# Optimization experiments

Measured on AMD Instinct MI355X. Metric: run time of the kernel, lower is better.

## Reference

```python
import jax, jax.numpy as jnp
import numpy as np

HIDDEN = 512
B, N = 32, 96

def setup_inputs() -> dict:
    key = jax.random.key(0)
    k1, k2, k3, k4, k5 = jax.random.split(key, 5)
    h = HIDDEN
    s1 = 1.0 / np.sqrt(2 * h)
    s2 = 1.0 / np.sqrt(h)
    return {
        "encoded_sequence": jax.random.normal(k1, (B, N, h), dtype=jnp.float32),
        "W1": jax.random.uniform(k2, (h, 2 * h), dtype=jnp.float32, minval=-s1, maxval=s1),
        "b1": jax.random.uniform(k3, (h,), dtype=jnp.float32, minval=-s1, maxval=s1),
        "W2": jax.random.uniform(k4, (1, h), dtype=jnp.float32, minval=-s2, maxval=s2),
        "b2": jax.random.uniform(k5, (1,), dtype=jnp.float32, minval=-s2, maxval=s2),
    }

def reference(encoded_sequence, W1, b1, W2, b2):
    # Faithful to calc_arc_scores: arc_vectors[b,i,j] = concat(X[b,i], X[b,j]),
    # scores = Linear2(tanh(Linear1(arc_vectors))).squeeze(-1).
    # Fused (biaffine) form: split W1 into head/dep halves and broadcast-sum,
    # avoiding the O(B*n^2*2h) concatenated intermediate.
    h = W1.shape[0]
    X = encoded_sequence
    Wa = W1[:, :h]   # acts on X_i (first half of concat)
    Wb = W1[:, h:]   # acts on X_j (second half of concat)
    Ha = jnp.einsum('bnh,kh->bnk', X, Wa)            # [B, n, h]
    Hb = jnp.einsum('bnh,kh->bnk', X, Wb)            # [B, n, h]
    T = jnp.tanh(Ha[:, :, None, :] + Hb[:, None, :, :] + b1)  # [B, n, n, h]
    arc_scores = jnp.einsum('bijk,k->bij', T, W2[0]) + b2[0]   # [B, n, n]
    return arc_scores
```

## Files before the change

### kernel.cpp

```cpp
#include <hip/hip_runtime.h>
#include <hip/hip_bf16.h>

#define NN 96
#define C_TANH 2.8853900817779268f

typedef __attribute__((ext_vector_type(4))) float    f32x4;
typedef __attribute__((ext_vector_type(2))) float    f32x2;
typedef __attribute__((ext_vector_type(8))) short    short8;
typedef __attribute__((ext_vector_type(8))) _Float16 half8;

static __device__ inline unsigned int cvt_pk_bf16(float lo, float hi) {
    unsigned int r;
    asm("v_cvt_pk_bf16_f32 %0, %1, %2" : "=v"(r) : "v"(lo), "v"(hi));
    return r;
}

__global__ __launch_bounds__(256) void gemm_h(const float* __restrict__ X,
                                              const float* __restrict__ W1,
                                              const float* __restrict__ b1,
                                              _Float16* __restrict__ Ea,
                                              _Float16* __restrict__ Eh) {
    __shared__ unsigned short As[2][2048];
    __shared__ unsigned short Bs[2][2048];

    int bid  = blockIdx.x;
    int xcd  = bid & 7;
    int sub  = bid >> 3;
    int mloc = sub % 6;
    int nq   = sub / 6;
    int mb   = (xcd * 6 + mloc) * 64;
    int nb   = nq * 64;
    int tid = threadIdx.x;
    int w   = tid >> 6;
    int l   = tid & 63;

    int srow = tid >> 2;
    int sg   = (tid & 3) * 8;
    int scs  = sg ^ ((srow & 3) << 3);
    const float* asrc = X + (mb + srow) * 512 + sg;
    int nrow = nb + srow;
    const float* bsrc = W1 + (nrow & 511) * 1024 + ((nrow >> 9) << 9) + sg;
    unsigned short* adst = &As[0][srow * 32 + scs];
    unsigned short* bdst = &Bs[0][srow * 32 + scs];

    struct Regs { f32x4 a0, a1, b0, b4; };
    Regs RA, RB;

#define LOADR(R, k0)                                                          \
    {                                                                         \
        R.a0 = *(const f32x4*)(asrc + (k0));                                  \
        R.a1 = *(const f32x4*)(asrc + (k0) + 4);                              \
        R.b0 = *(const f32x4*)(bsrc + (k0));                                  \
        R.b4 = *(const f32x4*)(bsrc + (k0) + 4);                              \
    }
#define WRITER(R, buf)                                                        \
    {                                                                         \
        uint4 ua, ub;                                                         \
        ua.x = cvt_pk_bf16(R.a0[0], R.a0[1]); ua.y = cvt_pk_bf16(R.a0[2], R.a0[3]); \
        ua.z = cvt_pk_bf16(R.a1[0], R.a1[1]); ua.w = cvt_pk_bf16(R.a1[2], R.a1[3]); \
        ub.x = cvt_pk_bf16(R.b0[0], R.b0[1]); ub.y = cvt_pk_bf16(R.b0[2], R.b0[3]); \
        ub.z = cvt_pk_bf16(R.b4[0], R.b4[1]); ub.w = cvt_pk_bf16(R.b4[2], R.b4[3]); \
        *(uint4*)(adst + (buf) * 2048) = ua;                                  \
        *(uint4*)(bdst + (buf) * 2048) = ub;                                  \
    }

    int lr    = l & 15;
    int koffs = ((l >> 4) * 8) ^ ((lr & 3) << 3);
    int aoff  = (16 * w + lr) * 32 + koffs;
    int boff0 = lr * 32 + koffs;

    f32x4 acc[4] = {};

#define COMPUTE(cur)                                                          \
    {                                                                         \
        short8 afr = *(const short8*)(&As[cur][aoff]);                        \
        short8 bfr[4];                                                        \
        _Pragma("unroll")                                                     \
        for (int t = 0; t < 4; ++t)                                           \
            bfr[t] = *(const short8*)(&Bs[cur][boff0 + t * 512]);             \
        _Pragma("unroll")                                                     \
        for (int t = 0; t < 4; ++t)                                           \
            acc[t] = __builtin_amdgcn_mfma_f32_16x16x32_bf16(afr, bfr[t],     \
                                                             acc[t], 0, 0, 0);\
    }

    LOADR(RA, 0)
    WRITER(RA, 0)
    LOADR(RB, 32)
    __syncthreads();
#pragma unroll 1
    for (int kk = 0; kk < 7; ++kk) {
        LOADR(RA, (2 * kk + 2) * 32)
        COMPUTE(0)
        WRITER(RB, 1)
        __syncthreads();
        LOADR(RB, (2 * kk + 3) * 32)
        COMPUTE(1)
        WRITER(RA, 0)
        __syncthreads();
    }
    COMPUTE(0)
    WRITER(RB, 1)
    __syncthreads();
    COMPUTE(1)
#undef LOADR
#undef WRITER
#undef COMPUTE

    int r0 = (l >> 4) * 4;
    bool isB = (nb >= 512);
    int colbase = nb & 511;
    _Float16* dst = isB ? Eh : Ea;
#pragma unroll
    for (int t = 0; t < 4; ++t) {
        int col = colbase + 16 * t + lr;
        float bias = isB ? b1[col] : 0.0f;
#pragma unroll
        for (int q = 0; q < 4; ++q) {
            int m = mb + 16 * w + r0 + q;
            float arg = (acc[t][q] + bias) * C_TANH;
            dst[m * 512 + col] = (_Float16)exp2f(arg);
        }
    }
}

__global__ __launch_bounds__(256) void arc_kernel(const _Float16* __restrict__ Ea,
                                                  const _Float16* __restrict__ Eh,
                                                  const float* __restrict__ w2,
                                                  const float* __restrict__ b2,
                                                  float* __restrict__ out) {
    __shared__ _Float16 a_s[16 * 512];
    __shared__ _Float16 h_s[16 * 512];
    __shared__ float    red[3][64][4];

    int bid = blockIdx.x;
    int xcd = bid & 7;
    int sub = bid >> 3;
    int b   = xcd * 4 + sub / 36;
    int r   = sub % 36;
    int it  = r / 6;
    int jt  = r % 6;
    int tid = threadIdx.x;

    const _Float16* asrc = Ea + (b * NN + it * 16) * 512;
    const _Float16* hsrc = Eh + (b * NN + jt * 16) * 512;

#pragma unroll
    for (int p = 0; p < 4; ++p) {
        int idx = tid + p * 256;
        int row = idx >> 6, c = idx & 63;
        int cs = c ^ (row & 7);
        *(f32x4*)(a_s + row * 512 + cs * 8) = *(const f32x4*)(asrc + row * 512 + c * 8);
        *(f32x4*)(h_s + row * 512 + cs * 8) = *(const f32x4*)(hsrc + row * 512 + c * 8);
    }
    __syncthreads();

    int w  = tid >> 6;
    int kq = __builtin_amdgcn_readfirstlane(w);
    int l  = tid & 63;
    int pi = l >> 3;
    int pj = l & 7;
    int r0a = pi * 2, r1a = r0a + 1;
    int r0h = pj * 2, r1h = r0h + 1;

    const _Float16* a0 = a_s + r0a * 512 + kq * 128;
    const _Float16* a1 = a_s + r1a * 512 + kq * 128;
    const _Float16* h0 = h_s + r0h * 512 + kq * 128;
    const _Float16* h1 = h_s + r1h * 512 + kq * 128;
    int sa0 = r0a & 7, sa1 = r1a & 7, sh0 = r0h & 7, sh1 = r1h & 7;
    const float* wp = w2 + kq * 128;

    float acc00 = 0.f, acc01 = 0.f, acc10 = 0.f, acc11 = 0.f;

#define PROC(av, hv, acc)                                                     \
    {                                                                         \
        float s0 = __builtin_fmaf((float)av[0], (float)hv[0], 1.0f);          \
        float s1 = __builtin_fmaf((float)av[1], (float)hv[1], 1.0f);          \
        float s2 = __builtin_fmaf((float)av[2], (float)hv[2], 1.0f);          \
        float s3 = __builtin_fmaf((float)av[3], (float)hv[3], 1.0f);          \
        float s4 = __builtin_fmaf((float)av[4], (float)hv[4], 1.0f);          \
        float s5 = __builtin_fmaf((float)av[5], (float)hv[5], 1.0f);          \
        float s6 = __builtin_fmaf((float)av[6], (float)hv[6], 1.0f);          \
        float s7 = __builtin_fmaf((float)av[7], (float)hv[7], 1.0f);          \
        float n0 = __builtin_fmaf(wv1, s0, wv0 * s1);                         \
        float n1 = __builtin_fmaf(wv3, s2, wv2 * s3);                         \
        float n2 = __builtin_fmaf(wv5, s4, wv4 * s5);                         \
        float n3 = __builtin_fmaf(wv7, s6, wv6 * s7);                         \
        acc = __builtin_fmaf(n0, __builtin_amdgcn_rcpf(s0 * s1), acc);        \
        acc = __builtin_fmaf(n1, __builtin_amdgcn_rcpf(s2 * s3), acc);        \
        acc = __builtin_fmaf(n2, __builtin_amdgcn_rcpf(s4 * s5), acc);        \
        acc = __builtin_fmaf(n3, __builtin_amdgcn_rcpf(s6 * s7), acc);        \
    }

#pragma unroll 4
    for (int c = 0; c < 16; ++c) {
        half8 av0 = *(const half8*)(a0 + ((c ^ sa0) << 3));
        half8 av1 = *(const half8*)(a1 + ((c ^ sa1) << 3));
        half8 hv0 = *(const half8*)(h0 + ((c ^ sh0) << 3));
        half8 hv1 = *(const half8*)(h1 + ((c ^ sh1) << 3));
        f32x4 wlo = *(const f32x4*)(wp + c * 8);
        f32x4 whi = *(const f32x4*)(wp + c * 8 + 4);
        float wv0 = wlo[0], wv1 = wlo[1], wv2 = wlo[2], wv3 = wlo[3];
        float wv4 = whi[0], wv5 = whi[1], wv6 = whi[2], wv7 = whi[3];
        PROC(av0, hv0, acc00)
        PROC(av0, hv1, acc01)
        PROC(av1, hv0, acc10)
        PROC(av1, hv1, acc11)
    }
#undef PROC

    if (w != 0) {
        f32x4 v = {acc00, acc01, acc10, acc11};
        *(f32x4*)(&red[w - 1][l][0]) = v;
    }
    __syncthreads();

    if (w == 0) {
#pragma unroll
        for (int rr = 0; rr < 3; ++rr) {
            f32x4 v = *(const f32x4*)(&red[rr][l][0]);
            acc00 += v[0]; acc01 += v[1]; acc10 += v[2]; acc11 += v[3];
        }
        f32x4 v0 = *(const f32x4*)(w2 + l * 8);
        f32x4 v1 = *(const f32x4*)(w2 + l * 8 + 4);
        float sv = (v0[0] + v0[1]) + (v0[2] + v0[3])
                 + (v1[0] + v1[1]) + (v1[2] + v1[3]);
#pragma unroll
        for (int off = 32; off; off >>= 1) sv += __shfl_xor(sv, off, 64);
        float Sv = sv + b2[0];

        int i0 = it * 16 + r0a;
        int j0 = jt * 16 + r0h;
        f32x2 o0 = {__builtin_fmaf(-2.f, acc00, Sv), __builtin_fmaf(-2.f, acc01, Sv)};
        f32x2 o1 = {__builtin_fmaf(-2.f, acc10, Sv), __builtin_fmaf(-2.f, acc11, Sv)};
        *(f32x2*)(out + (b * NN + i0) * NN + j0)     = o0;
        *(f32x2*)(out + (b * NN + i0 + 1) * NN + j0) = o1;
    }
}

extern "C" void kernel_launch(void* const* d_in, const int* in_sizes, int n_in,
                              void* d_out, int out_size, void* d_ws, size_t ws_size,
                              hipStream_t stream) {
    (void)in_sizes; (void)n_in; (void)out_size; (void)ws_size;

    const float* X  = (const float*)d_in[0];
    const float* W1 = (const float*)d_in[1];
    const float* b1 = (const float*)d_in[2];
    const float* W2 = (const float*)d_in[3];
    const float* b2 = (const float*)d_in[4];
    float* out = (float*)d_out;

    char* ws = (char*)d_ws;
    _Float16* Ea = (_Float16*)(ws);
    _Float16* Eh = (_Float16*)(ws + 3145728);

    gemm_h<<<768, 256, 0, stream>>>(X, W1, b1, Ea, Eh);
    arc_kernel<<<1152, 256, 0, stream>>>(Ea, Eh, W2, b2, out);
}
```

Measured before the change: 35.83 us.

## Pre-convert X and W1 to swizzled bf16 in a separate kernel before GEMM

Adds a cvt_swz kernel that converts X and the rearranged W1 to bf16 once, writing them in the LDS swizzle order to a workspace. The GEMM then loads half as many bytes per tile and copies them straight into shared memory with no per-tile conversion. This removes the repeated fp32 loads and conversions of the same rows across GEMM blocks, but adds a third kernel launch and an extra round trip through global memory.

```diff
diff --git a/kernel.cpp b/kernel.cpp
--- a/kernel.cpp
+++ b/kernel.cpp
@@ -4,10 +4,11 @@
 #define NN 96
 #define C_TANH 2.8853900817779268f
 
-typedef __attribute__((ext_vector_type(4))) float    f32x4;
-typedef __attribute__((ext_vector_type(2))) float    f32x2;
-typedef __attribute__((ext_vector_type(8))) short    short8;
-typedef __attribute__((ext_vector_type(8))) _Float16 half8;
+typedef __attribute__((ext_vector_type(4))) float        f32x4;
+typedef __attribute__((ext_vector_type(2))) float        f32x2;
+typedef __attribute__((ext_vector_type(8))) short        short8;
+typedef __attribute__((ext_vector_type(8))) _Float16     half8;
+typedef __attribute__((ext_vector_type(4))) unsigned int u32x4;
 
 static __device__ inline unsigned int cvt_pk_bf16(float lo, float hi) {
     unsigned int r;
@@ -15,8 +16,35 @@
     return r;
 }
 
-__global__ __launch_bounds__(256) void gemm_h(const float* __restrict__ X,
-                                              const float* __restrict__ W1,
+__global__ __launch_bounds__(256) void cvt_swz(const float* __restrict__ X,
+                                               const float* __restrict__ W1,
+                                               unsigned short* __restrict__ Xb,
+                                               unsigned short* __restrict__ Wb) {
+    int idx = blockIdx.x * 256 + threadIdx.x;
+    const float* src;
+    unsigned short* dst;
+    if (idx < 196608) {
+        int r = idx >> 6, c = idx & 63;
+        int sc = (c & ~3) | ((c & 3) ^ (r & 3));
+        src = X + r * 512 + sc * 8;
+        dst = Xb + r * 512 + c * 8;
+    } else {
+        int i2 = idx - 196608;
+        int n = i2 >> 6, c = i2 & 63;
+        int sc = (c & ~3) | ((c & 3) ^ (n & 3));
+        src = W1 + (n & 511) * 1024 + ((n >> 9) << 9) + sc * 8;
+        dst = Wb + n * 512 + c * 8;
+    }
+    f32x4 f0 = *(const f32x4*)(src);
+    f32x4 f1 = *(const f32x4*)(src + 4);
+    u32x4 u;
+    u.x = cvt_pk_bf16(f0[0], f0[1]); u.y = cvt_pk_bf16(f0[2], f0[3]);
+    u.z = cvt_pk_bf16(f1[0], f1[1]); u.w = cvt_pk_bf16(f1[2], f1[3]);
+    *(u32x4*)dst = u;
+}
+
+__global__ __launch_bounds__(256) void gemm_h(const unsigned short* __restrict__ Xb,
+                                              const unsigned short* __restrict__ Wb,
                                               const float* __restrict__ b1,
                                               _Float16* __restrict__ Ea,
                                               _Float16* __restrict__ Eh) {
@@ -36,32 +64,21 @@
 
     int srow = tid >> 2;
     int sg   = (tid & 3) * 8;
-    int scs  = sg ^ ((srow & 3) << 3);
-    const float* asrc = X + (mb + srow) * 512 + sg;
-    int nrow = nb + srow;
-    const float* bsrc = W1 + (nrow & 511) * 1024 + ((nrow >> 9) << 9) + sg;
-    unsigned short* adst = &As[0][srow * 32 + scs];
-    unsigned short* bdst = &Bs[0][srow * 32 + scs];
-
-    struct Regs { f32x4 a0, a1, b0, b4; };
-    Regs RA, RB;
-
-#define LOADR(R, k0)                                                          \
-    {                                                                         \
-        R.a0 = *(const f32x4*)(asrc + (k0));                                  \
-        R.a1 = *(const f32x4*)(asrc + (k0) + 4);                              \
-        R.b0 = *(const f32x4*)(bsrc + (k0));                                  \
-        R.b4 = *(const f32x4*)(bsrc + (k0) + 4);                              \
-    }
-#define WRITER(R, buf)                                                        \
-    {                                                                         \
-        uint4 ua, ub;                                                         \
-        ua.x = cvt_pk_bf16(R.a0[0], R.a0[1]); ua.y = cvt_pk_bf16(R.a0[2], R.a0[3]); \
-        ua.z = cvt_pk_bf16(R.a1[0], R.a1[1]); ua.w = cvt_pk_bf16(R.a1[2], R.a1[3]); \
-        ub.x = cvt_pk_bf16(R.b0[0], R.b0[1]); ub.y = cvt_pk_bf16(R.b0[2], R.b0[3]); \
-        ub.z = cvt_pk_bf16(R.b4[0], R.b4[1]); ub.w = cvt_pk_bf16(R.b4[2], R.b4[3]); \
-        *(uint4*)(adst + (buf) * 2048) = ua;                                  \
-        *(uint4*)(bdst + (buf) * 2048) = ub;                                  \
+    const unsigned short* asrc = Xb + (mb + srow) * 512 + sg;
+    const unsigned short* bsrc = Wb + (nb + srow) * 512 + sg;
+    unsigned short* adst = &As[0][srow * 32 + sg];
+    unsigned short* bdst = &Bs[0][srow * 32 + sg];
+
+    u32x4 RAa, RAb, RBa, RBb;
+#define LOADR(Ra, Rb, k0)                                                     \
+    {                                                                         \
+        Ra = *(const u32x4*)(asrc + (k0));                                    \
+        Rb = *(const u32x4*)(bsrc + (k0));                                    \
+    }
+#define WRITER(Ra, Rb, buf)                                                   \
+    {                                                                         \
+        *(u32x4*)(adst + (buf) * 2048) = Ra;                                  \
+        *(u32x4*)(bdst + (buf) * 2048) = Rb;                                  \
     }
 
     int lr    = l & 15;
@@ -84,23 +101,23 @@
                                                              acc[t], 0, 0, 0);\
     }
 
-    LOADR(RA, 0)
-    WRITER(RA, 0)
-    LOADR(RB, 32)
+    LOADR(RAa, RAb, 0)
+    WRITER(RAa, RAb, 0)
+    LOADR(RBa, RBb, 32)
     __syncthreads();
 #pragma unroll 1
     for (int kk = 0; kk < 7; ++kk) {
-        LOADR(RA, (2 * kk + 2) * 32)
+        LOADR(RAa, RAb, (2 * kk + 2) * 32)
         COMPUTE(0)
-        WRITER(RB, 1)
+        WRITER(RBa, RBb, 1)
         __syncthreads();
-        LOADR(RB, (2 * kk + 3) * 32)
+        LOADR(RBa, RBb, (2 * kk + 3) * 32)
         COMPUTE(1)
-        WRITER(RA, 0)
+        WRITER(RAa, RAb, 0)
         __syncthreads();
     }
     COMPUTE(0)
-    WRITER(RB, 1)
+    WRITER(RBa, RBb, 1)
     __syncthreads();
     COMPUTE(1)
 #undef LOADR
@@ -251,9 +268,12 @@
     float* out = (float*)d_out;
 
     char* ws = (char*)d_ws;
-    _Float16* Ea = (_Float16*)(ws);
-    _Float16* Eh = (_Float16*)(ws + 3145728);
-
-    gemm_h<<<768, 256, 0, stream>>>(X, W1, b1, Ea, Eh);
+    unsigned short* Xb = (unsigned short*)(ws);
+    unsigned short* Wb = (unsigned short*)(ws + 3145728);
+    _Float16* Ea = (_Float16*)(ws + 4194304);
+    _Float16* Eh = (_Float16*)(ws + 7340032);
+
+    cvt_swz<<<1024, 256, 0, stream>>>(X, W1, Xb, Wb);
+    gemm_h<<<768, 256, 0, stream>>>(Xb, Wb, b1, Ea, Eh);
     arc_kernel<<<1152, 256, 0, stream>>>(Ea, Eh, W2, b2, out);
 }
```

New measurement: 39.62 us. 1.11x slower.
